# Optimization experiments

Measured on AMD Instinct MI355X. Metric: run time of the kernel, lower is better.

The kernel has to match this reference:

```python
import jax, jax.numpy as jnp
import numpy as np

LBDA = 0.5  # soft-min temperature, matches OTAM_cum_dist_v2 default


def setup_inputs() -> dict:
    key = jax.random.key(0)
    # frame distance scores (e.g. 1 - cosine similarity), in [0, 2]
    dists = jax.random.uniform(key, (200, 200, 32, 32), dtype=jnp.float32) * 2.0
    return {"dists": dists}


def _otam_cum_dist(dists, lbda=LBDA):
    """Faithful translation of OTAM_cum_dist_v2.

    dists: [Q, S, L, M] -> returns cum_dists[:, :, -1, -1] of shape [Q, S].
    The torch code pads the last dim by (1,1) with zeros, does a cumulative
    sum along row 0, and for each subsequent row a serial soft-min
    (-lbda * log(sum(exp(-x/lbda)))) recurrence along columns. Column 0 is
    never written and stays 0. Columns m==1 and m==Mp-1 include an extra
    diagonal/above term prev_row[m]; interior columns use only prev_row[m-1]
    and the running value cum[l, m-1].
    """
    Q, S, L, M = dists.shape
    Mp = M + 2
    # pad last dim by one zero on each side, move (L, Mp) to the front
    d = jnp.pad(dists, ((0, 0), (0, 0), (0, 0), (1, 1)))
    d = jnp.transpose(d, (2, 3, 0, 1))  # [L, Mp, Q, S]

    # row 0: cum[0, m] = cum[0, m-1] + d[0, m]; d[0,0]=0 so plain cumsum works
    row0 = jnp.cumsum(d[0], axis=0)  # [Mp, Q, S]

    m_idx = jnp.arange(1, Mp)
    mask3 = (m_idx == 1) | (m_idx == Mp - 1)  # columns with the 3-term soft-min

    def row_step(prev_row, d_row):
        # prev_row, d_row: [Mp, Q, S]
        def col_step(c, xs):
            d_m, p_m1, p_m, m3 = xs
            # soft-min: -lbda * log( exp(-p_m1/l) + exp(-c/l) [+ exp(-p_m/l)] )
            s = jnp.logaddexp(-p_m1 / lbda, -c / lbda)
            s = jnp.where(m3, jnp.logaddexp(s, -p_m / lbda), s)
            v = d_m - lbda * s
            return v, v

        xs = (d_row[1:], prev_row[:-1], prev_row[1:], mask3)
        _, vals = jax.lax.scan(col_step, jnp.zeros_like(d_row[0]), xs)
        new_row = jnp.concatenate([jnp.zeros_like(vals[:1]), vals], axis=0)
        return new_row, 0.0

    last_row, _ = jax.lax.scan(row_step, row0, d[1:])
    return last_row[-1]  # cum_dists[:, :, -1, -1] -> [Q, S]


def reference(dists):
    return _otam_cum_dist(dists, LBDA)
```

## Files before the change

kernel.cpp:

```cpp
#include <hip/hip_runtime.h>
#include <math.h>


constexpr int QS = 40000;
constexpr int PPB = 8;

__device__ __forceinline__ float wave_shr1(float v) {
    int r = __builtin_amdgcn_update_dpp(0, __builtin_bit_cast(int, v),
                                        0x138 , 0xF, 0xF, true);
    return __builtin_bit_cast(float, r);
}

__global__ __launch_bounds__(256) void otam_wavefront(const float* __restrict__ dists,
                                                      float* __restrict__ out) {
    __shared__ float lds[PPB * 1024];
    const int tid = threadIdx.x;
    const int blockP0 = blockIdx.x * PPB;

    {
        const float4* src = (const float4*)(dists + (size_t)blockP0 * 1024);
        float4* dst = (float4*)lds;
#pragma unroll
        for (int i = 0; i < 8; ++i)
            dst[tid + 256 * i] = src[tid + 256 * i];
    }
    __syncthreads();

    const int lane = tid & 63;
    const int l = lane & 31;
    const int pl = (tid >> 6) * 2 + (lane >> 5);
    const bool l0 = (l == 0);
    const float* base = lds + pl * 1024 + 31 * l;

    const float BIG = 1e30f;
    const float K = -2.8853900817779268f;
    const float C2 = -0.34657359027997264f;

    float myval = 0.f;
    float pm1 = l0 ? BIG : 0.f;

#pragma unroll
    for (int t = 1; t <= 64; ++t) {
        float pm = wave_shr1(myval);
        int m = t - l;
        float dval = (t < 64) ? base[t - 1] : 0.f;
        float dm = ((unsigned)(m - 1) < 32u) ? dval : 0.f;
        bool m3 = (m == 1) || (m == 33);
        float x3 = (m3 && !l0) ? pm : BIG;
        float p1 = l0 ? BIG : pm1;
        float mn = fminf(fminf(p1, myval), x3);
        float nkmn = -K * mn;
        float e1 = __builtin_amdgcn_exp2f(fmaf(K, p1, nkmn));
        float e2 = __builtin_amdgcn_exp2f(fmaf(K, myval, nkmn));
        float e3 = __builtin_amdgcn_exp2f(fmaf(K, x3, nkmn));
        float s = e1 + e2 + e3;
        float v = fmaf(C2, __builtin_amdgcn_logf(s), dm + mn);
        bool active = ((unsigned)(m - 1) < 33u);
        myval = active ? v : myval;
        pm1 = pm;
    }

    if (l == 31) out[blockP0 + pl] = myval;
}

extern "C" void kernel_launch(void* const* d_in, const int* in_sizes, int n_in,
                              void* d_out, int out_size, void* d_ws, size_t ws_size,
                              hipStream_t stream) {
    const float* dists = (const float*)d_in[0];
    float* out = (float*)d_out;
    dim3 grid(QS / PPB);
    dim3 block(256);
    hipLaunchKernelGGL(otam_wavefront, grid, block, 0, stream, dists, out);
}
```

Measured before the change: 226.5 us.

## Stage distances as fp16 in LDS with rotated rows and register-resident row cache

Converts the input tile to half precision when staging it into shared memory. Each row is stored rotated by its row index so that the diagonal wavefront access pattern becomes a contiguous per-lane row, which is then loaded once into sixteen half2 registers. The per-step LDS reads go away and the active-mask select is dropped in favour of reset logic keyed on the column-1 and column-33 steps, with launch bounds raised to target higher occupancy. Storing the inputs as fp16 loses precision in the accumulated soft-min sums, and the larger register footprint may work against the occupancy hint.

New measurement: 232.1 us. +2.5%, slower.

```diff
diff --git a/kernel.cpp b/kernel.cpp
--- a/kernel.cpp
+++ b/kernel.cpp
@@ -1,4 +1,5 @@
 #include <hip/hip_runtime.h>
+#include <hip/hip_fp16.h>
 #include <math.h>
 
 
@@ -11,52 +12,71 @@
     return __builtin_bit_cast(float, r);
 }
 
-__global__ __launch_bounds__(256) void otam_wavefront(const float* __restrict__ dists,
-                                                      float* __restrict__ out) {
-    __shared__ float lds[PPB * 1024];
+__global__ __launch_bounds__(256, 8) void otam_wavefront(const float* __restrict__ dists,
+                                                         float* __restrict__ out) {
+    __shared__ __align__(16) __half lh[PPB * 1024];
     const int tid = threadIdx.x;
     const int blockP0 = blockIdx.x * PPB;
 
     {
         const float4* src = (const float4*)(dists + (size_t)blockP0 * 1024);
-        float4* dst = (float4*)lds;
 #pragma unroll
-        for (int i = 0; i < 8; ++i)
-            dst[tid + 256 * i] = src[tid + 256 * i];
+        for (int i = 0; i < 8; ++i) {
+            int f = tid + 256 * i;
+            float4 v = src[f];
+            int flat = f << 2;
+            int p = flat >> 10;
+            int r = (flat >> 5) & 31;
+            int e0 = flat & 31;
+            __half* row = &lh[(p << 10) + (r << 5)];
+            int rb = (e0 + r) & 31;
+            row[rb] = __float2half(v.x);
+            row[(rb + 1) & 31] = __float2half(v.y);
+            row[(rb + 2) & 31] = __float2half(v.z);
+            row[(rb + 3) & 31] = __float2half(v.w);
+        }
     }
     __syncthreads();
 
     const int lane = tid & 63;
     const int l = lane & 31;
-    const int pl = (tid >> 6) * 2 + (lane >> 5);
+    const int pl = ((tid >> 6) << 1) + (lane >> 5);
     const bool l0 = (l == 0);
-    const float* base = lds + pl * 1024 + 31 * l;
+
+    __half2 rh[16];
+    {
+        const __half2* rb2 = (const __half2*)&lh[(pl << 10) + (l << 5)];
+#pragma unroll
+        for (int k = 0; k < 16; ++k) rh[k] = rb2[k];
+    }
 
     const float BIG = 1e30f;
     const float K = -2.8853900817779268f;
     const float C2 = -0.34657359027997264f;
 
     float myval = 0.f;
-    float pm1 = l0 ? BIG : 0.f;
+    float pm1 = 0.f;
 
 #pragma unroll
     for (int t = 1; t <= 64; ++t) {
         float pm = wave_shr1(myval);
-        int m = t - l;
-        float dval = (t < 64) ? base[t - 1] : 0.f;
-        float dm = ((unsigned)(m - 1) < 32u) ? dval : 0.f;
-        bool m3 = (m == 1) || (m == 33);
-        float x3 = (m3 && !l0) ? pm : BIG;
-        float p1 = l0 ? BIG : pm1;
-        float mn = fminf(fminf(p1, myval), x3);
-        float nkmn = -K * mn;
-        float e1 = __builtin_amdgcn_exp2f(fmaf(K, p1, nkmn));
-        float e2 = __builtin_amdgcn_exp2f(fmaf(K, myval, nkmn));
-        float e3 = __builtin_amdgcn_exp2f(fmaf(K, x3, nkmn));
+        int j = (t - 1) & 31;
+        __half2 hp = rh[j >> 1];
+        float dval = (j & 1) ? __high2float(hp) : __low2float(hp);
+        bool m1 = (l == t - 1);
+        bool m33 = (l == t - 33);
+        float dm = m33 ? 0.f : dval;
+        float c = m1 ? 0.f : myval;
+        float p1 = m1 ? 0.f : pm1;
+        p1 = l0 ? BIG : p1;
+        float x3 = ((m1 | m33) & (int)!l0) ? pm : BIG;
+        float mn = fminf(fminf(p1, c), x3);
+        float nk = -K * mn;
+        float e1 = __builtin_amdgcn_exp2f(fmaf(K, p1, nk));
+        float e2 = __builtin_amdgcn_exp2f(fmaf(K, c, nk));
+        float e3 = __builtin_amdgcn_exp2f(fmaf(K, x3, nk));
         float s = e1 + e2 + e3;
-        float v = fmaf(C2, __builtin_amdgcn_logf(s), dm + mn);
-        bool active = ((unsigned)(m - 1) < 33u);
-        myval = active ? v : myval;
+        myval = fmaf(C2, __builtin_amdgcn_logf(s), dm + mn);
         pm1 = pm;
     }
 
```
